# Optimization experiments

Measured on AMD Instinct MI355X. Metric: run time of the kernel, lower is better.

Reference implementation:

```python
import jax, jax.numpy as jnp
import numpy as np

N, C, T, V, K = 64, 64, 300, 25, 3
EPS = 1e-5


def setup_inputs() -> dict:
    key = jax.random.key(0)
    ks = jax.random.split(key, 4)
    x = jax.random.normal(ks[0], (N, C, T, V), dtype=jnp.float32)
    A = jax.random.uniform(ks[1], (K, V, V), dtype=jnp.float32)
    # per-subset 1x1 conv weights: W[k] maps C_in -> C_out, plus bias b[k]
    W = jax.random.normal(ks[2], (K, C, C), dtype=jnp.float32) * (1.0 / np.sqrt(C))
    b = jax.random.normal(ks[3], (K, C), dtype=jnp.float32) * 0.01
    gamma = jnp.ones((C,), dtype=jnp.float32)
    beta = jnp.zeros((C,), dtype=jnp.float32)
    return {"x": x, "A": A, "W": W, "b": b, "gamma": gamma, "beta": beta}


def reference(x, A, W, b, gamma, beta):
    # y = sum_k conv1x1_k( einsum('nctv,vw->nctw', x, A[k]) )
    # conv1x1 over (C,T,V) with kernel 1 == channel matmul; fuse subsets via one einsum.
    y = jnp.einsum('nctv,kvw,koc->notw', x, A, W)
    y = y + jnp.sum(b, axis=0)[None, :, None, None]
    # BatchNorm2d in training mode: batch statistics over (N, T, V) per channel
    mean = jnp.mean(y, axis=(0, 2, 3), keepdims=True)
    var = jnp.mean(jnp.square(y - mean), axis=(0, 2, 3), keepdims=True)
    y = gamma[None, :, None, None] * (y - mean) * jax.lax.rsqrt(var + EPS) + beta[None, :, None, None]
    # residual (in_channels == out_channels -> identity) + relu
    return jax.nn.relu(y + x)
```

## Files before the change

### kernel.cpp

```cpp
#include <hip/hip_runtime.h>
#include <hip/hip_bf16.h>

#define N_ 64
#define C_ 64
#define T_ 300
#define V_ 25
#define K_ 3
#define TT 12
#define NTILE 25
#define NBLK 1600
#define NPERS 800
#define XROW 384
#define WP 72
#define ATP 40
#define NTHR 512
#define EPS_ 1e-5f

typedef __bf16 bf16_t;
typedef __bf16 bf16x4 __attribute__((ext_vector_type(4)));
typedef __bf16 bf16x8 __attribute__((ext_vector_type(8)));
typedef float f32x4 __attribute__((ext_vector_type(4)));
typedef float f32x4u __attribute__((ext_vector_type(4), aligned(4)));

static __device__ __forceinline__ bf16_t tobf(float f) { return (bf16_t)f; }
static __device__ __forceinline__ int emask(int c) { return ((c & 3) << 3) | ((c & 8) << 2); }

union SmemU {
  struct { bf16_t W[3 * 64 * WP]; bf16_t At[3 * 32 * ATP]; } wa;
  bf16_t xs[64 * XROW];
};

struct Frags {
  bf16x8 wfrag[6];
  bf16x8 afrag[3][2];
  int fK[4], fS5[4];
  float bs[4];
  int obase;
};

static __device__ __forceinline__ void stage_wa(
    const float* __restrict__ A, const float* __restrict__ W, SmemU& sm, int tid) {
  for (int m = tid; m < 3072; m += NTHR) {
    f32x4 v4 = *(reinterpret_cast<const f32x4*>(W) + m);
    int f = m << 2;
    int k = f >> 12, o = (f >> 6) & 63, c = f & 63;
    bf16x4 h;
    h[0] = tobf(v4[0]); h[1] = tobf(v4[1]); h[2] = tobf(v4[2]); h[3] = tobf(v4[3]);
    *reinterpret_cast<bf16x4*>(&sm.wa.W[(k * 64 + o) * WP + c]) = h;
  }
  for (int i = tid; i < 3072; i += NTHR) {
    int k = i >> 10, r = i & 1023, w = r >> 5, v = r & 31;
    float val = (v < V_ && w < V_) ? A[k * 625 + v * 25 + w] : 0.f;
    sm.wa.At[(k * 32 + w) * ATP + v] = tobf(val);
  }
}

static __device__ __forceinline__ void read_frags(
    const SmemU& sm, const float* __restrict__ b, int ob, int l15, int lg, Frags& F) {
  const int o = ob * 16 + l15;
  #pragma unroll
  for (int k = 0; k < 3; ++k)
    #pragma unroll
    for (int ch = 0; ch < 2; ++ch)
      F.wfrag[k * 2 + ch] =
          *reinterpret_cast<const bf16x8*>(&sm.wa.W[(k * 64 + o) * WP + ch * 32 + lg * 8]);
  #pragma unroll
  for (int k = 0; k < 3; ++k)
    #pragma unroll
    for (int wh = 0; wh < 2; ++wh)
      F.afrag[k][wh] =
          *reinterpret_cast<const bf16x8*>(&sm.wa.At[(k * 32 + wh * 16 + l15) * ATP + lg * 8]);
  const int crow = 8 * (l15 >> 2) + (l15 & 3);
  #pragma unroll
  for (int q = 0; q < 4; ++q) {
    int c = ((q >> 1) * 32) + ((q & 1) * 4) + crow;
    int em = emask(c);
    F.fK[q] = c * XROW + ((lg * 8) ^ (em & 24));
    F.fS5[q] = em & 32;
  }
  F.obase = ob * 16 + lg * 4;
  #pragma unroll
  for (int r = 0; r < 4; ++r)
    F.bs[r] = b[F.obase + r] + b[64 + F.obase + r] + b[128 + F.obase + r];
}

static __device__ __forceinline__ void touch_issue(
    const float* __restrict__ x, int tile, int tid, float* tv) {
  const int n = tile / NTILE;
  const int t0 = (tile - n * NTILE) * TT;
  const float* base = x + (size_t)n * 480000 + (size_t)t0 * 25;
  #pragma unroll
  for (int j = 0; j < 3; ++j) {
    int idx = tid + (j << 9);
    int c = idx / 19;
    int li = idx - c * 19;
    tv[j] = (c < 64) ? base[(size_t)c * 7500 + li * 16] : 0.f;
  }
}

static __device__ __forceinline__ void stage_x(
    const float* __restrict__ x, SmemU& sm, int n, int t0, int tid) {
  const int c = tid >> 3, vb = tid & 7;
  const int em = emask(c);
  const float* xr = x + (size_t)n * 480000 + (size_t)c * 7500 + (size_t)t0 * 25;
  bf16_t* xsr = &sm.xs[c * XROW];
  #pragma unroll
  for (int t = 0; t < TT; ++t) {
    bf16x4 h;
    if (vb < 6) {
      f32x4u v4 = *reinterpret_cast<const f32x4u*>(xr + t * 25 + vb * 4);
      h[0] = tobf(v4[0]); h[1] = tobf(v4[1]); h[2] = tobf(v4[2]); h[3] = tobf(v4[3]);
    } else if (vb == 6) {
      float s = xr[t * 25 + 24];
      h[0] = tobf(s); h[1] = tobf(0.f); h[2] = tobf(0.f); h[3] = tobf(0.f);
    } else {
      h[0] = tobf(0.f); h[1] = tobf(0.f); h[2] = tobf(0.f); h[3] = tobf(0.f);
    }
    *reinterpret_cast<bf16x4*>(&xsr[(((t << 5) + vb * 4) ^ em)]) = h;
  }
}

static __device__ __forceinline__ void compute_wh(
    const bf16x8* xf, const Frags& F, int wh, f32x4& acc0, f32x4& acc1) {
  acc0 = f32x4{0.f, 0.f, 0.f, 0.f};
  acc1 = f32x4{0.f, 0.f, 0.f, 0.f};
  #pragma unroll
  for (int k = 0; k < 3; ++k) {
    #pragma unroll
    for (int ch = 0; ch < 2; ++ch) {
      f32x4 zero = {0.f, 0.f, 0.f, 0.f};
      f32x4 dP = __builtin_amdgcn_mfma_f32_16x16x32_bf16(xf[ch * 2 + 0], F.afrag[k][wh], zero, 0, 0, 0);
      f32x4 dQ = __builtin_amdgcn_mfma_f32_16x16x32_bf16(xf[ch * 2 + 1], F.afrag[k][wh], zero, 0, 0, 0);
      bf16x8 zf;
      zf[0] = tobf(dP[0]); zf[1] = tobf(dP[1]); zf[2] = tobf(dP[2]); zf[3] = tobf(dP[3]);
      zf[4] = tobf(dQ[0]); zf[5] = tobf(dQ[1]); zf[6] = tobf(dQ[2]); zf[7] = tobf(dQ[3]);
      if (ch == 0)
        acc0 = __builtin_amdgcn_mfma_f32_16x16x32_bf16(F.wfrag[k * 2 + ch], zf, acc0, 0, 0, 0);
      else
        acc1 = __builtin_amdgcn_mfma_f32_16x16x32_bf16(F.wfrag[k * 2 + ch], zf, acc1, 0, 0, 0);
    }
  }
}

__global__ __launch_bounds__(NTHR, 4) void k1_compute(
    const float* __restrict__ x, const float* __restrict__ A,
    const float* __restrict__ W, const float* __restrict__ b,
    float* __restrict__ y, float* __restrict__ part) {
  __shared__ __align__(16) SmemU sm;
  __shared__ float stats2[2][2][64];

  const int bid = blockIdx.x;
  const int tid = threadIdx.x;
  const int lane = tid & 63;
  const int wv = tid >> 6;
  const int ob = wv & 3;
  const int th = wv >> 2;
  const int l15 = lane & 15;
  const int lg = lane >> 4;

  stage_wa(A, W, sm, tid);
  __syncthreads();
  Frags F;
  read_frags(sm, b, ob, l15, lg, F);
  __syncthreads();

  float lsum[4] = {0.f, 0.f, 0.f, 0.f}, lsq[4] = {0.f, 0.f, 0.f, 0.f};
  float sink = 0.f;

  #pragma unroll
  for (int i = 0; i < 2; ++i) {
    const int tile = bid * 2 + i;
    const int n = tile / NTILE;
    const int t0 = (tile - n * NTILE) * TT;

    stage_x(x, sm, n, t0, tid);
    __syncthreads();

    float tv[3] = {0.f, 0.f, 0.f};
    if (i == 0) touch_issue(x, tile + 1, tid, tv);

    float* yb = y + (size_t)n * 480000 + (size_t)t0 * 25;

    #pragma unroll 2
    for (int tl = 0; tl < 6; ++tl) {
      const int t = th * 6 + tl;
      bf16x8 xf[4];
      #pragma unroll
      for (int q = 0; q < 4; ++q)
        xf[q] = *reinterpret_cast<const bf16x8*>(sm.xs + F.fK[q] + ((t << 5) ^ F.fS5[q]));
      #pragma unroll
      for (int wh = 0; wh < 2; ++wh) {
        f32x4 acc0, acc1;
        compute_wh(xf, F, wh, acc0, acc1);
        const int w = wh ? 16 + l15 : l15;
        if (w < V_) {
          #pragma unroll
          for (int r = 0; r < 4; ++r) {
            float val = acc0[r] + acc1[r] + F.bs[r];
            lsum[r] += val;
            lsq[r] += val * val;
            yb[(size_t)(F.obase + r) * 7500 + t * 25 + w] = val;
          }
        }
      }
    }
    sink += tv[0] + tv[1] + tv[2];
    __syncthreads();
  }
  asm volatile("" :: "v"(sink));

  #pragma unroll
  for (int d = 1; d < 16; d <<= 1) {
    #pragma unroll
    for (int r = 0; r < 4; ++r) {
      lsum[r] += __shfl_xor(lsum[r], d);
      lsq[r]  += __shfl_xor(lsq[r], d);
    }
  }
  if (l15 == 0) {
    #pragma unroll
    for (int r = 0; r < 4; ++r) {
      stats2[0][th][F.obase + r] = lsum[r];
      stats2[1][th][F.obase + r] = lsq[r];
    }
  }
  __syncthreads();
  if (tid < 128)
    part[(size_t)bid * 128 + tid] =
        stats2[tid >> 6][0][tid & 63] + stats2[tid >> 6][1][tid & 63];
}

__global__ __launch_bounds__(256) void k2_stats(
    const float* __restrict__ part,
    const float* __restrict__ gamma, const float* __restrict__ beta,
    float* __restrict__ ss) {
  const int o = blockIdx.x;
  const int tid = threadIdx.x;
  double s = 0.0, q = 0.0;
  for (int i = tid; i < NPERS; i += 256) {
    s += (double)part[(size_t)i * 128 + o];
    q += (double)part[(size_t)i * 128 + 64 + o];
  }
  __shared__ double sd[256], qd[256];
  sd[tid] = s; qd[tid] = q;
  __syncthreads();
  for (int step = 128; step > 0; step >>= 1) {
    if (tid < step) { sd[tid] += sd[tid + step]; qd[tid] += qd[tid + step]; }
    __syncthreads();
  }
  if (tid == 0) {
    const double cnt = 480000.0;
    double mean = sd[0] / cnt;
    double var = qd[0] / cnt - mean * mean;
    float inv = rsqrtf((float)var + EPS_);
    float sc = gamma[o] * inv;
    float sh = beta[o] - (float)mean * sc;
    ss[2 * o] = sc;
    ss[2 * o + 1] = sh;
  }
}

__global__ __launch_bounds__(256) void k3_finish(
    const float* __restrict__ x, const float* __restrict__ ss,
    float* __restrict__ y) {
  const int p = blockIdx.x;
  const int c = p & 63;
  const float sc = ss[2 * c];
  const float sh = ss[2 * c + 1];
  const f32x4* xv = reinterpret_cast<const f32x4*>(x + (size_t)p * 7500);
  f32x4* yv = reinterpret_cast<f32x4*>(y + (size_t)p * 7500);
  for (int i = threadIdx.x; i < 1875; i += 256) {
    f32x4 a = yv[i];
    f32x4 b4 = xv[i];
    f32x4 o;
    o[0] = fmaxf(sc * a[0] + sh + b4[0], 0.f);
    o[1] = fmaxf(sc * a[1] + sh + b4[1], 0.f);
    o[2] = fmaxf(sc * a[2] + sh + b4[2], 0.f);
    o[3] = fmaxf(sc * a[3] + sh + b4[3], 0.f);
    __builtin_nontemporal_store(o, yv + i);
  }
}

extern "C" void kernel_launch(void* const* d_in, const int* in_sizes, int n_in,
                              void* d_out, int out_size, void* d_ws, size_t ws_size,
                              hipStream_t stream) {
  const float* x     = (const float*)d_in[0];
  const float* A     = (const float*)d_in[1];
  const float* W     = (const float*)d_in[2];
  const float* b     = (const float*)d_in[3];
  const float* gamma = (const float*)d_in[4];
  const float* beta  = (const float*)d_in[5];
  float* y = (float*)d_out;

  float* part = (float*)d_ws;
  float* ss   = part + (size_t)NPERS * 128;

  k1_compute<<<NPERS, NTHR, 0, stream>>>(x, A, W, b, y, part);
  k2_stats<<<64, 256, 0, stream>>>(part, gamma, beta, ss);
  k3_finish<<<4096, 256, 0, stream>>>(x, ss, y);
}
```

Before: 141.9 us.

## Stage pre-BN output as bf16 in workspace with fragment-native layout

```diff
diff --git a/kernel.cpp b/kernel.cpp
--- a/kernel.cpp
+++ b/kernel.cpp
@@ -15,6 +15,7 @@
 #define ATP 40
 #define NTHR 512
 #define EPS_ 1e-5f
+#define YELEMS ((size_t)64 * 300 * 4 * 512)
 
 typedef __bf16 bf16_t;
 typedef __bf16 bf16x4 __attribute__((ext_vector_type(4)));
@@ -142,10 +143,12 @@
   }
 }
 
+template<int MODE>
 __global__ __launch_bounds__(NTHR, 4) void k1_compute(
     const float* __restrict__ x, const float* __restrict__ A,
     const float* __restrict__ W, const float* __restrict__ b,
-    float* __restrict__ y, float* __restrict__ part) {
+    float* __restrict__ y, bf16_t* __restrict__ ystage,
+    float* __restrict__ part) {
   __shared__ __align__(16) SmemU sm;
   __shared__ float stats2[2][2][64];
 
@@ -199,8 +202,21 @@
             float val = acc0[r] + acc1[r] + F.bs[r];
             lsum[r] += val;
             lsq[r] += val * val;
-            yb[(size_t)(F.obase + r) * 7500 + t * 25 + w] = val;
           }
+        }
+        if constexpr (MODE == 0) {
+          if (w < V_) {
+            #pragma unroll
+            for (int r = 0; r < 4; ++r)
+              yb[(size_t)(F.obase + r) * 7500 + t * 25 + w] =
+                  acc0[r] + acc1[r] + F.bs[r];
+          }
+        } else {
+          bf16_t* cb = ystage + (size_t)(n * 300 + t0 + t) * 2048 +
+                       ob * 512 + wh * 256 + lane;
+          #pragma unroll
+          for (int r = 0; r < 4; ++r)
+            cb[r * 64] = tobf(acc0[r] + acc1[r] + F.bs[r]);
         }
       }
     }
@@ -281,6 +297,40 @@
   }
 }
 
+__global__ __launch_bounds__(256) void k3_finish_ws(
+    const float* __restrict__ x, const bf16_t* __restrict__ ystage,
+    const float* __restrict__ ss, float* __restrict__ out) {
+  __shared__ bf16_t ys[300 * 32];
+  const int p = blockIdx.x;
+  const int n = p >> 6, o = p & 63;
+  const int ob = o >> 4, lg = (o >> 2) & 3, r = o & 3;
+  const float sc = ss[2 * o], sh = ss[2 * o + 1];
+
+  const bf16_t* ybase = ystage + (size_t)n * 300 * 2048 + ob * 512 + r * 64 + lg * 16;
+  for (int idx = threadIdx.x; idx < 300 * 32; idx += 256) {
+    int t = idx >> 5, w = idx & 31;
+    ys[idx] = ybase[(size_t)t * 2048 + (w >> 4) * 256 + (w & 15)];
+  }
+  __syncthreads();
+
+  const float* xp = x + (size_t)p * 7500;
+  float* op = out + (size_t)p * 7500;
+  for (int i = threadIdx.x; i < 1875; i += 256) {
+    int e = 4 * i;
+    f32x4u xv4 = *reinterpret_cast<const f32x4u*>(xp + e);
+    f32x4 ov;
+    #pragma unroll
+    for (int j = 0; j < 4; ++j) {
+      int ej = e + j;
+      int t = ej / 25;
+      int w = ej - t * 25;
+      float yv = (float)ys[t * 32 + w];
+      ov[j] = fmaxf(sc * yv + sh + xv4[j], 0.f);
+    }
+    __builtin_nontemporal_store(ov, reinterpret_cast<f32x4*>(op + e));
+  }
+}
+
 extern "C" void kernel_launch(void* const* d_in, const int* in_sizes, int n_in,
                               void* d_out, int out_size, void* d_ws, size_t ws_size,
                               hipStream_t stream) {
@@ -290,12 +340,21 @@
   const float* b     = (const float*)d_in[3];
   const float* gamma = (const float*)d_in[4];
   const float* beta  = (const float*)d_in[5];
-  float* y = (float*)d_out;
-
-  float* part = (float*)d_ws;
-  float* ss   = part + (size_t)NPERS * 128;
-
-  k1_compute<<<NPERS, NTHR, 0, stream>>>(x, A, W, b, y, part);
-  k2_stats<<<64, 256, 0, stream>>>(part, gamma, beta, ss);
-  k3_finish<<<4096, 256, 0, stream>>>(x, ss, y);
-}
+  float* out = (float*)d_out;
+
+  const size_t need = YELEMS * 2 + (size_t)NPERS * 128 * 4 + 512;
+  if (ws_size >= need) {
+    bf16_t* ystage = (bf16_t*)d_ws;
+    float* part = (float*)((char*)d_ws + YELEMS * 2);
+    float* ss   = part + (size_t)NPERS * 128;
+    k1_compute<1><<<NPERS, NTHR, 0, stream>>>(x, A, W, b, nullptr, ystage, part);
+    k2_stats<<<64, 256, 0, stream>>>(part, gamma, beta, ss);
+    k3_finish_ws<<<4096, 256, 0, stream>>>(x, ystage, ss, out);
+  } else {
+    float* part = (float*)d_ws;
+    float* ss   = part + (size_t)NPERS * 128;
+    k1_compute<0><<<NPERS, NTHR, 0, stream>>>(x, A, W, b, out, nullptr, part);
+    k2_stats<<<64, 256, 0, stream>>>(part, gamma, beta, ss);
+    k3_finish<<<4096, 256, 0, stream>>>(x, ss, out);
+  }
+}
```

New measurement: 142.3 us. About the same (+0.3%).
